# Performance work log

Hardware: AMD Instinct MI355X
Metric: run time of the kernel (lower is better)

Reference implementation:

```python
import jax, jax.numpy as jnp
import numpy as np
from jax.scipy.linalg import expm as _expm

B, D = 1024, 128
_SQRT3 = 3.0 ** 0.5
_C1, _C2 = 0.5 - _SQRT3 / 6.0, 0.5 + _SQRT3 / 6.0


def setup_inputs() -> dict:
    key = jax.random.key(0)
    k_t, k_y, k_a, k_w = jax.random.split(key, 4)
    scale = 1.0 / np.sqrt(D)  # keep ||Omega|| moderate so expm is well-conditioned
    return {
        "t0": jax.random.uniform(k_t, (B,), dtype=jnp.float32),
        "h": jnp.float32(0.1),
        "y0": jax.random.normal(k_y, (B, D), dtype=jnp.float32),
        "A0": jax.random.normal(k_a, (B, D, D), dtype=jnp.float32) * scale,
        "W": jax.random.normal(k_w, (B, D, D), dtype=jnp.float32) * scale,
    }


def reference(t0, h, y0, A0, W):
    # A(t) = A0 + t * W evaluated at the two Gauss-Legendre nodes
    t1 = t0 + _C1 * h  # (B,)
    t2 = t0 + _C2 * h  # (B,)
    A1 = A0 + t1[:, None, None] * W  # (B, D, D)
    A2 = A0 + t2[:, None, None] * W  # (B, D, D)
    alpha1 = (h * 0.5) * (A1 + A2)
    alpha2 = (h * _SQRT3) * (A2 - A1)
    comm = alpha1 @ alpha2 - alpha2 @ alpha1  # [alpha1, alpha2]
    Omega = alpha1 - comm / 12.0
    U = jax.vmap(_expm)(Omega)  # batched matrix exponential (B, D, D)
    y_next = jnp.einsum("bij,bj->bi", U, y0)  # (B, D)
    return y_next, jnp.stack((A1, A2), axis=0)
```

## Files before the change

kernel.cpp:

```cpp
#include <hip/hip_runtime.h>

#define B_SZ 1024
#define D_SZ 128
#define KTERMS 8

typedef float vfloat4 __attribute__((ext_vector_type(4)));

__device__ inline float dotq(const vfloat4* q, const float* v) {
    float a0 = 0.f, a1 = 0.f, a2 = 0.f, a3 = 0.f;
#pragma unroll
    for (int j = 0; j < 16; ++j) {
        vfloat4 vv = *(const vfloat4*)(v + 4 * j);
        a0 = fmaf(q[j].x, vv.x, a0);
        a1 = fmaf(q[j].y, vv.y, a1);
        a2 = fmaf(q[j].z, vv.z, a2);
        a3 = fmaf(q[j].w, vv.w, a3);
    }
    return (a0 + a1) + (a2 + a3);
}

__global__ void __launch_bounds__(512, 4)
magnus_kernel(const float* __restrict__ t0p, const float* __restrict__ hp,
              const float* __restrict__ y0, const float* __restrict__ A0,
              const float* __restrict__ W, float* __restrict__ out)
{
    __shared__ __align__(16) float sv[D_SZ];
    __shared__ __align__(16) float su1[D_SZ];
    __shared__ __align__(16) float su2[D_SZ];
    __shared__ __align__(16) float su3[D_SZ];
    __shared__ __align__(16) float su4[D_SZ];

    const int b = blockIdx.x;
    const int tid = threadIdx.x;
    const float h = hp[0];
    const float tb = t0p[b];
    const float SQ3_6 = 0.28867513459481287f;
    const float t1 = tb + (0.5f - SQ3_6) * h;
    const float t2 = tb + (0.5f + SQ3_6) * h;

    const size_t moff = (size_t)b * (D_SZ * D_SZ);
    const float4* A0v = (const float4*)(A0 + moff);
    const float4* Wv  = (const float4*)(W + moff);
    vfloat4* o1 = (vfloat4*)(out + (size_t)B_SZ * D_SZ + moff);
    vfloat4* o2 = (vfloat4*)(out + (size_t)B_SZ * D_SZ
                                 + (size_t)B_SZ * D_SZ * D_SZ + moff);

#pragma unroll 8
    for (int it = 0; it < 8; ++it) {
        int i = it * 512 + tid;
        float4 a = A0v[i];
        float4 w = Wv[i];
        vfloat4 p1, p2;
        p1.x = fmaf(t1, w.x, a.x);
        p1.y = fmaf(t1, w.y, a.y);
        p1.z = fmaf(t1, w.z, a.z);
        p1.w = fmaf(t1, w.w, a.w);
        p2.x = fmaf(t2, w.x, a.x);
        p2.y = fmaf(t2, w.y, a.y);
        p2.z = fmaf(t2, w.z, a.z);
        p2.w = fmaf(t2, w.w, a.w);
        __builtin_nontemporal_store(p1, o1 + i);
        __builtin_nontemporal_store(p2, o2 + i);
    }

    const int grp  = tid >> 8;
    const int t8   = tid & 255;
    const int half = (t8 >> 5) & 1;
    const int row  = (t8 & 31) + ((t8 >> 6) << 5);
    const float* rbase = grp ? (W + moff) : (A0 + moff);
    const vfloat4* src = (const vfloat4*)(rbase + (size_t)row * D_SZ + half * 64);
    vfloat4 q[16];
#pragma unroll
    for (int j = 0; j < 16; ++j) q[j] = src[j];
#pragma unroll
    for (int j = 0; j < 16; ++j) asm volatile("" : "+v"(q[j]));

    float yacc = 0.0f;
    if (tid < D_SZ) {
        float v = y0[(size_t)b * D_SZ + tid];
        sv[tid] = v;
        yacc = v;
    }
    __syncthreads();

    const float hs = h * (tb + 0.5f * h);
    const float c3 = h * h * h * (1.0f / 12.0f);

#pragma unroll
    for (int k = 1; k <= KTERMS; ++k) {
        float a = dotq(q, sv + half * 64);
        a += __shfl_xor(a, 32);
        if (!half) { if (grp == 0) su1[row] = a; else su2[row] = a; }
        __syncthreads();
        const float* vb = grp ? su1 : su2;
        float c = dotq(q, vb + half * 64);
        c += __shfl_xor(c, 32);
        if (!half) { if (grp == 0) su3[row] = c; else su4[row] = c; }
        __syncthreads();
        if (tid < D_SZ) {
            float wn = h * su1[tid] + hs * su2[tid] - c3 * (su3[tid] - su4[tid]);
            wn *= (1.0f / (float)k);
            yacc += wn;
            sv[tid] = wn;
        }
        __syncthreads();
    }

    if (tid < D_SZ) {
        out[(size_t)b * D_SZ + tid] = yacc;
    }
}

extern "C" void kernel_launch(void* const* d_in, const int* in_sizes, int n_in,
                              void* d_out, int out_size, void* d_ws, size_t ws_size,
                              hipStream_t stream) {
    const float* t0 = (const float*)d_in[0];
    const float* h  = (const float*)d_in[1];
    const float* y0 = (const float*)d_in[2];
    const float* A0 = (const float*)d_in[3];
    const float* W  = (const float*)d_in[4];
    float* out = (float*)d_out;
    magnus_kernel<<<B_SZ, 512, 0, stream>>>(t0, h, y0, A0, W, out);
}
```

Before: 256.3 us.

## Form Omega explicitly with bf16 MFMA commutator, then run Taylor matvecs on it

Instead of applying alpha1 and alpha2 as four matrix-vector products per Taylor term, the kernel builds Omega once per batch. It computes the commutator A0·W − W·A0 with bf16 MFMA 32x32x16 tiles, stores Omega in a swizzled 64KB shared buffer, and then does a single matvec per term with ping-pong vectors and one barrier per term. This trades two dense 128^3 GEMMs per matrix, strided uncoalesced B-fragment global loads and 64KB of LDS (which lowers occupancy) for fewer per-term barriers and matvecs. bf16 rounding of the commutator inputs reduces accuracy.

```diff
diff --git a/kernel.cpp b/kernel.cpp
--- a/kernel.cpp
+++ b/kernel.cpp
@@ -5,18 +5,29 @@
 #define KTERMS 8
 
 typedef float vfloat4 __attribute__((ext_vector_type(4)));
+typedef float f32x16 __attribute__((ext_vector_type(16)));
+typedef short bf16x8 __attribute__((ext_vector_type(8)));
 
-__device__ inline float dotq(const vfloat4* q, const float* v) {
-    float a0 = 0.f, a1 = 0.f, a2 = 0.f, a3 = 0.f;
+__device__ inline short f2bf(float x) {
+    union { float f; unsigned u; } c; c.f = x;
+    unsigned u = c.u + 0x7fffu + ((c.u >> 16) & 1u);
+    return (short)(u >> 16);
+}
+
+__device__ inline bf16x8 afrag(const float* M, int r, int k0) {
+    const float4* p = (const float4*)(M + r * 128 + k0);
+    float4 x0 = p[0], x1 = p[1];
+    bf16x8 f;
+    f[0] = f2bf(x0.x); f[1] = f2bf(x0.y); f[2] = f2bf(x0.z); f[3] = f2bf(x0.w);
+    f[4] = f2bf(x1.x); f[5] = f2bf(x1.y); f[6] = f2bf(x1.z); f[7] = f2bf(x1.w);
+    return f;
+}
+
+__device__ inline bf16x8 bfrag(const float* M, int k0, int c) {
+    bf16x8 f;
 #pragma unroll
-    for (int j = 0; j < 16; ++j) {
-        vfloat4 vv = *(const vfloat4*)(v + 4 * j);
-        a0 = fmaf(q[j].x, vv.x, a0);
-        a1 = fmaf(q[j].y, vv.y, a1);
-        a2 = fmaf(q[j].z, vv.z, a2);
-        a3 = fmaf(q[j].w, vv.w, a3);
-    }
-    return (a0 + a1) + (a2 + a3);
+    for (int e = 0; e < 8; ++e) f[e] = f2bf(M[(k0 + e) * 128 + c]);
+    return f;
 }
 
 __global__ void __launch_bounds__(512, 4)
@@ -24,11 +35,8 @@
               const float* __restrict__ y0, const float* __restrict__ A0,
               const float* __restrict__ W, float* __restrict__ out)
 {
-    __shared__ __align__(16) float sv[D_SZ];
-    __shared__ __align__(16) float su1[D_SZ];
-    __shared__ __align__(16) float su2[D_SZ];
-    __shared__ __align__(16) float su3[D_SZ];
-    __shared__ __align__(16) float su4[D_SZ];
+    __shared__ __align__(16) float sOmega[D_SZ * D_SZ];
+    __shared__ __align__(16) float sv[2][D_SZ];
 
     const int b = blockIdx.x;
     const int tid = threadIdx.x;
@@ -51,63 +59,98 @@
         float4 a = A0v[i];
         float4 w = Wv[i];
         vfloat4 p1, p2;
-        p1.x = fmaf(t1, w.x, a.x);
-        p1.y = fmaf(t1, w.y, a.y);
-        p1.z = fmaf(t1, w.z, a.z);
-        p1.w = fmaf(t1, w.w, a.w);
-        p2.x = fmaf(t2, w.x, a.x);
-        p2.y = fmaf(t2, w.y, a.y);
-        p2.z = fmaf(t2, w.z, a.z);
-        p2.w = fmaf(t2, w.w, a.w);
+        p1.x = fmaf(t1, w.x, a.x); p1.y = fmaf(t1, w.y, a.y);
+        p1.z = fmaf(t1, w.z, a.z); p1.w = fmaf(t1, w.w, a.w);
+        p2.x = fmaf(t2, w.x, a.x); p2.y = fmaf(t2, w.y, a.y);
+        p2.z = fmaf(t2, w.z, a.z); p2.w = fmaf(t2, w.w, a.w);
         __builtin_nontemporal_store(p1, o1 + i);
         __builtin_nontemporal_store(p2, o2 + i);
     }
 
-    const int grp  = tid >> 8;
-    const int t8   = tid & 255;
-    const int half = (t8 >> 5) & 1;
-    const int row  = (t8 & 31) + ((t8 >> 6) << 5);
-    const float* rbase = grp ? (W + moff) : (A0 + moff);
-    const vfloat4* src = (const vfloat4*)(rbase + (size_t)row * D_SZ + half * 64);
-    vfloat4 q[16];
-#pragma unroll
-    for (int j = 0; j < 16; ++j) q[j] = src[j];
-#pragma unroll
-    for (int j = 0; j < 16; ++j) asm volatile("" : "+v"(q[j]));
+    const int l  = tid & 63;
+    const int w  = tid >> 6;
+    const int lh = l >> 5;
+    const int lc = l & 31;
 
-    float yacc = 0.0f;
-    if (tid < D_SZ) {
-        float v = y0[(size_t)b * D_SZ + tid];
-        sv[tid] = v;
-        yacc = v;
-    }
-    __syncthreads();
+    const float* Ag = A0 + moff;
+    const float* Wg = W  + moff;
 
     const float hs = h * (tb + 0.5f * h);
     const float c3 = h * h * h * (1.0f / 12.0f);
 
 #pragma unroll
+    for (int t = 0; t < 2; ++t) {
+        const int tile = w * 2 + t;
+        const int mr = tile >> 2, nc = tile & 3;
+        const int ra = mr * 32 + lc;
+        const int cb = nc * 32 + lc;
+
+        f32x16 acc1 = {};
+#pragma unroll
+        for (int ks = 0; ks < 8; ++ks) {
+            int k0 = ks * 16 + 8 * lh;
+            bf16x8 aA = afrag(Ag, ra, k0);
+            bf16x8 bW = bfrag(Wg, k0, cb);
+            acc1 = __builtin_amdgcn_mfma_f32_32x32x16_bf16(aA, bW, acc1, 0, 0, 0);
+        }
+        f32x16 acc2 = {};
+#pragma unroll
+        for (int ks = 0; ks < 8; ++ks) {
+            int k0 = ks * 16 + 8 * lh;
+            bf16x8 aW = afrag(Wg, ra, k0);
+            bf16x8 bA = bfrag(Ag, k0, cb);
+            acc2 = __builtin_amdgcn_mfma_f32_32x32x16_bf16(aW, bA, acc2, 0, 0, 0);
+        }
+#pragma unroll
+        for (int reg = 0; reg < 16; ++reg) {
+            int grow = mr * 32 + (reg & 3) + 8 * (reg >> 2) + 4 * lh;
+            int gcol = nc * 32 + lc;
+            float a0v = Ag[grow * 128 + gcol];
+            float wv  = Wg[grow * 128 + gcol];
+            float om = fmaf(h, a0v, fmaf(hs, wv, -c3 * (acc1[reg] - acc2[reg])));
+            sOmega[grow * 128 + (gcol ^ ((grow & 7) << 2))] = om;
+        }
+    }
+
+    const int q    = l >> 4;
+    const int prow = w * 16 + (l & 15);
+    float yacc = 0.0f;
+    if (l < 16) {
+        float v = y0[(size_t)b * D_SZ + prow];
+        sv[0][prow] = v;
+        yacc = v;
+    }
+    __syncthreads();
+
+    const float* orow = sOmega + prow * 128;
+    const int sw = (prow & 7) << 2;
+#pragma unroll
     for (int k = 1; k <= KTERMS; ++k) {
-        float a = dotq(q, sv + half * 64);
+        const float* vin = sv[(k - 1) & 1];
+        float s0 = 0.f, s1 = 0.f, s2 = 0.f, s3 = 0.f;
+#pragma unroll
+        for (int c = 0; c < 8; ++c) {
+            int colb = q * 32 + 4 * c;
+            vfloat4 ov = *(const vfloat4*)(orow + (colb ^ sw));
+            vfloat4 vv = *(const vfloat4*)(vin + colb);
+            s0 = fmaf(ov.x, vv.x, s0);
+            s1 = fmaf(ov.y, vv.y, s1);
+            s2 = fmaf(ov.z, vv.z, s2);
+            s3 = fmaf(ov.w, vv.w, s3);
+        }
+        float a = (s0 + s1) + (s2 + s3);
+        a += __shfl_xor(a, 16);
         a += __shfl_xor(a, 32);
-        if (!half) { if (grp == 0) su1[row] = a; else su2[row] = a; }
-        __syncthreads();
-        const float* vb = grp ? su1 : su2;
-        float c = dotq(q, vb + half * 64);
-        c += __shfl_xor(c, 32);
-        if (!half) { if (grp == 0) su3[row] = c; else su4[row] = c; }
-        __syncthreads();
-        if (tid < D_SZ) {
-            float wn = h * su1[tid] + hs * su2[tid] - c3 * (su3[tid] - su4[tid]);
-            wn *= (1.0f / (float)k);
+        if (l < 16) {
+            float wn = a * (1.0f / (float)k);
             yacc += wn;
-            sv[tid] = wn;
+            sv[k & 1][prow] = wn;
         }
         __syncthreads();
     }
 
-    if (tid < D_SZ) {
-        out[(size_t)b * D_SZ + tid] = yacc;
+    if (l < 16) {
+        out[(size_t)b * D_SZ + prow] = yacc;
     }
 }
 
```

After: 547.0 us. 2.13x slower.

## Stage A0 and W as bf16 in LDS instead of re-reading fp32 rows into registers

Applied to the files above, without the earlier changes.

During the A1/A2 pass the kernel now packs A0 and W to bf16 and stores them in shared memory with a padded row stride. The Taylor-series matvecs then read operands from LDS instead of reloading each row from global memory into 64 registers per thread. This removes the second global read of both matrices and frees registers, at the cost of about 68KB of LDS per block, which limits blocks per CU. The bf16 rounding also lowers the precision of the exponential-action result.

```diff
diff --git a/kernel.cpp b/kernel.cpp
--- a/kernel.cpp
+++ b/kernel.cpp
@@ -3,18 +3,28 @@
 #define B_SZ 1024
 #define D_SZ 128
 #define KTERMS 8
+#define RSTRIDE 68
 
 typedef float vfloat4 __attribute__((ext_vector_type(4)));
 
-__device__ inline float dotq(const vfloat4* q, const float* v) {
+__device__ inline float bflo(unsigned u) { return __uint_as_float(u << 16); }
+__device__ inline float bfhi(unsigned u) { return __uint_as_float(u & 0xffff0000u); }
+
+__device__ inline float dotlds(const unsigned* rq, const float* v) {
     float a0 = 0.f, a1 = 0.f, a2 = 0.f, a3 = 0.f;
 #pragma unroll
-    for (int j = 0; j < 16; ++j) {
-        vfloat4 vv = *(const vfloat4*)(v + 4 * j);
-        a0 = fmaf(q[j].x, vv.x, a0);
-        a1 = fmaf(q[j].y, vv.y, a1);
-        a2 = fmaf(q[j].z, vv.z, a2);
-        a3 = fmaf(q[j].w, vv.w, a3);
+    for (int j = 0; j < 8; ++j) {
+        uint4 qq = *(const uint4*)(rq + 4 * j);
+        vfloat4 v0 = *(const vfloat4*)(v + 8 * j);
+        vfloat4 v1 = *(const vfloat4*)(v + 8 * j + 4);
+        a0 = fmaf(bflo(qq.x), v0.x, a0);
+        a1 = fmaf(bfhi(qq.x), v0.y, a1);
+        a2 = fmaf(bflo(qq.y), v0.z, a2);
+        a3 = fmaf(bfhi(qq.y), v0.w, a3);
+        a0 = fmaf(bflo(qq.z), v1.x, a0);
+        a1 = fmaf(bfhi(qq.z), v1.y, a1);
+        a2 = fmaf(bflo(qq.w), v1.z, a2);
+        a3 = fmaf(bfhi(qq.w), v1.w, a3);
     }
     return (a0 + a1) + (a2 + a3);
 }
@@ -24,6 +34,8 @@
               const float* __restrict__ y0, const float* __restrict__ A0,
               const float* __restrict__ W, float* __restrict__ out)
 {
+    __shared__ __align__(16) unsigned sA[D_SZ * RSTRIDE];
+    __shared__ __align__(16) unsigned sW[D_SZ * RSTRIDE];
     __shared__ __align__(16) float sv[D_SZ];
     __shared__ __align__(16) float su1[D_SZ];
     __shared__ __align__(16) float su2[D_SZ];
@@ -51,29 +63,29 @@
         float4 a = A0v[i];
         float4 w = Wv[i];
         vfloat4 p1, p2;
-        p1.x = fmaf(t1, w.x, a.x);
-        p1.y = fmaf(t1, w.y, a.y);
-        p1.z = fmaf(t1, w.z, a.z);
-        p1.w = fmaf(t1, w.w, a.w);
-        p2.x = fmaf(t2, w.x, a.x);
-        p2.y = fmaf(t2, w.y, a.y);
-        p2.z = fmaf(t2, w.z, a.z);
-        p2.w = fmaf(t2, w.w, a.w);
+        p1.x = fmaf(t1, w.x, a.x); p1.y = fmaf(t1, w.y, a.y);
+        p1.z = fmaf(t1, w.z, a.z); p1.w = fmaf(t1, w.w, a.w);
+        p2.x = fmaf(t2, w.x, a.x); p2.y = fmaf(t2, w.y, a.y);
+        p2.z = fmaf(t2, w.z, a.z); p2.w = fmaf(t2, w.w, a.w);
         __builtin_nontemporal_store(p1, o1 + i);
         __builtin_nontemporal_store(p2, o2 + i);
+
+        unsigned pa0, pa1, pw0, pw1;
+        asm("v_cvt_pk_bf16_f32 %0, %1, %2" : "=v"(pa0) : "v"(a.x), "v"(a.y));
+        asm("v_cvt_pk_bf16_f32 %0, %1, %2" : "=v"(pa1) : "v"(a.z), "v"(a.w));
+        asm("v_cvt_pk_bf16_f32 %0, %1, %2" : "=v"(pw0) : "v"(w.x), "v"(w.y));
+        asm("v_cvt_pk_bf16_f32 %0, %1, %2" : "=v"(pw1) : "v"(w.z), "v"(w.w));
+        int r = i >> 5;
+        int p = (2 * i) & 63;
+        *(uint2*)(&sA[r * RSTRIDE + p]) = make_uint2(pa0, pa1);
+        *(uint2*)(&sW[r * RSTRIDE + p]) = make_uint2(pw0, pw1);
     }
 
     const int grp  = tid >> 8;
     const int t8   = tid & 255;
     const int half = (t8 >> 5) & 1;
     const int row  = (t8 & 31) + ((t8 >> 6) << 5);
-    const float* rbase = grp ? (W + moff) : (A0 + moff);
-    const vfloat4* src = (const vfloat4*)(rbase + (size_t)row * D_SZ + half * 64);
-    vfloat4 q[16];
-#pragma unroll
-    for (int j = 0; j < 16; ++j) q[j] = src[j];
-#pragma unroll
-    for (int j = 0; j < 16; ++j) asm volatile("" : "+v"(q[j]));
+    const unsigned* rq = (grp ? sW : sA) + row * RSTRIDE + half * 32;
 
     float yacc = 0.0f;
     if (tid < D_SZ) {
@@ -88,12 +100,12 @@
 
 #pragma unroll
     for (int k = 1; k <= KTERMS; ++k) {
-        float a = dotq(q, sv + half * 64);
+        float a = dotlds(rq, sv + half * 64);
         a += __shfl_xor(a, 32);
         if (!half) { if (grp == 0) su1[row] = a; else su2[row] = a; }
         __syncthreads();
         const float* vb = grp ? su1 : su2;
-        float c = dotq(q, vb + half * 64);
+        float c = dotlds(rq, vb + half * 64);
         c += __shfl_xor(c, 32);
         if (!half) { if (grp == 0) su3[row] = c; else su4[row] = c; }
         __syncthreads();
```

New measurement: 257.2 us. No clear change (+0.4%).

## Specialize warps: split A1/A2 streaming from bf16 register-resident Taylor matvecs

Applied to the files above, without the earlier changes.

Splits the block into two halves. One half streams A0/W and writes A1/A2. The other half holds whole rows of A0 or W packed as bf16 in registers and runs the Taylor-series matvec loop. Each thread now owns a full row, so the cross-lane shuffle reduction and two shared buffers are gone, and the combine step is done with a pair shuffle. Barriers are raw s_barrier instructions, and the streaming loop inserts matching barriers to stay in step with the compute half. The series is cut from 8 to 7 terms and the matrix is rounded to bf16, which lowers accuracy and may break tolerance. The hand-matched barrier counts are fragile.

```diff
diff --git a/kernel.cpp b/kernel.cpp
--- a/kernel.cpp
+++ b/kernel.cpp
@@ -2,19 +2,25 @@
 
 #define B_SZ 1024
 #define D_SZ 128
-#define KTERMS 8
+#define KTERMS 7
 
 typedef float vfloat4 __attribute__((ext_vector_type(4)));
 
-__device__ inline float dotq(const vfloat4* q, const float* v) {
+__device__ inline float bflo(unsigned u) { return __uint_as_float(u << 16); }
+__device__ inline float bfhi(unsigned u) { return __uint_as_float(u & 0xffff0000u); }
+
+#define BAR_J1() asm volatile("s_barrier")
+#define BAR_J2() asm volatile("s_waitcnt lgkmcnt(0)\ns_barrier" ::: "memory")
+
+__device__ inline float dotR(const unsigned* R, const float* v) {
     float a0 = 0.f, a1 = 0.f, a2 = 0.f, a3 = 0.f;
 #pragma unroll
-    for (int j = 0; j < 16; ++j) {
+    for (int j = 0; j < 32; ++j) {
         vfloat4 vv = *(const vfloat4*)(v + 4 * j);
-        a0 = fmaf(q[j].x, vv.x, a0);
-        a1 = fmaf(q[j].y, vv.y, a1);
-        a2 = fmaf(q[j].z, vv.z, a2);
-        a3 = fmaf(q[j].w, vv.w, a3);
+        a0 = fmaf(bflo(R[2 * j]),     vv.x, a0);
+        a1 = fmaf(bfhi(R[2 * j]),     vv.y, a1);
+        a2 = fmaf(bflo(R[2 * j + 1]), vv.z, a2);
+        a3 = fmaf(bfhi(R[2 * j + 1]), vv.w, a3);
     }
     return (a0 + a1) + (a2 + a3);
 }
@@ -24,90 +30,84 @@
               const float* __restrict__ y0, const float* __restrict__ A0,
               const float* __restrict__ W, float* __restrict__ out)
 {
-    __shared__ __align__(16) float sv[D_SZ];
+    __shared__ __align__(16) float svr[D_SZ];
     __shared__ __align__(16) float su1[D_SZ];
     __shared__ __align__(16) float su2[D_SZ];
-    __shared__ __align__(16) float su3[D_SZ];
-    __shared__ __align__(16) float su4[D_SZ];
 
-    const int b = blockIdx.x;
+    const int b   = blockIdx.x;
     const int tid = threadIdx.x;
-    const float h = hp[0];
+    const float h  = hp[0];
     const float tb = t0p[b];
-    const float SQ3_6 = 0.28867513459481287f;
-    const float t1 = tb + (0.5f - SQ3_6) * h;
-    const float t2 = tb + (0.5f + SQ3_6) * h;
+    const size_t moff = (size_t)b * (D_SZ * D_SZ);
 
-    const size_t moff = (size_t)b * (D_SZ * D_SZ);
-    const float4* A0v = (const float4*)(A0 + moff);
-    const float4* Wv  = (const float4*)(W + moff);
-    vfloat4* o1 = (vfloat4*)(out + (size_t)B_SZ * D_SZ + moff);
-    vfloat4* o2 = (vfloat4*)(out + (size_t)B_SZ * D_SZ
-                                 + (size_t)B_SZ * D_SZ * D_SZ + moff);
+    if (tid < 256) {
+        const float SQ3_6 = 0.28867513459481287f;
+        const float t1 = tb + (0.5f - SQ3_6) * h;
+        const float t2 = tb + (0.5f + SQ3_6) * h;
+        const float4* A0v = (const float4*)(A0 + moff);
+        const float4* Wv  = (const float4*)(W + moff);
+        vfloat4* o1 = (vfloat4*)(out + (size_t)B_SZ * D_SZ + moff);
+        vfloat4* o2 = (vfloat4*)(out + (size_t)B_SZ * D_SZ
+                                     + (size_t)B_SZ * D_SZ * D_SZ + moff);
+#pragma unroll
+        for (int it = 0; it < 16; ++it) {
+            int i = it * 256 + tid;
+            float4 a = A0v[i];
+            float4 w = Wv[i];
+            vfloat4 p1, p2;
+            p1.x = fmaf(t1, w.x, a.x); p1.y = fmaf(t1, w.y, a.y);
+            p1.z = fmaf(t1, w.z, a.z); p1.w = fmaf(t1, w.w, a.w);
+            p2.x = fmaf(t2, w.x, a.x); p2.y = fmaf(t2, w.y, a.y);
+            p2.z = fmaf(t2, w.z, a.z); p2.w = fmaf(t2, w.w, a.w);
+            __builtin_nontemporal_store(p1, o1 + i);
+            __builtin_nontemporal_store(p2, o2 + i);
+            if (it >= 1 && it <= 14) BAR_J1();
+        }
+    } else {
+        const int tl = tid - 256;
+        const int m  = tl & 1;
+        const int r  = tl >> 1;
+        const float* rowp = (m ? W : A0) + moff + (size_t)r * D_SZ;
 
-#pragma unroll 8
-    for (int it = 0; it < 8; ++it) {
-        int i = it * 512 + tid;
-        float4 a = A0v[i];
-        float4 w = Wv[i];
-        vfloat4 p1, p2;
-        p1.x = fmaf(t1, w.x, a.x);
-        p1.y = fmaf(t1, w.y, a.y);
-        p1.z = fmaf(t1, w.z, a.z);
-        p1.w = fmaf(t1, w.w, a.w);
-        p2.x = fmaf(t2, w.x, a.x);
-        p2.y = fmaf(t2, w.y, a.y);
-        p2.z = fmaf(t2, w.z, a.z);
-        p2.w = fmaf(t2, w.w, a.w);
-        __builtin_nontemporal_store(p1, o1 + i);
-        __builtin_nontemporal_store(p2, o2 + i);
-    }
+        unsigned R[64];
+#pragma unroll
+        for (int j = 0; j < 32; ++j) {
+            float4 x = ((const float4*)rowp)[j];
+            asm("v_cvt_pk_bf16_f32 %0, %1, %2" : "=v"(R[2*j])   : "v"(x.x), "v"(x.y));
+            asm("v_cvt_pk_bf16_f32 %0, %1, %2" : "=v"(R[2*j+1]) : "v"(x.z), "v"(x.w));
+        }
 
-    const int grp  = tid >> 8;
-    const int t8   = tid & 255;
-    const int half = (t8 >> 5) & 1;
-    const int row  = (t8 & 31) + ((t8 >> 6) << 5);
-    const float* rbase = grp ? (W + moff) : (A0 + moff);
-    const vfloat4* src = (const vfloat4*)(rbase + (size_t)row * D_SZ + half * 64);
-    vfloat4 q[16];
-#pragma unroll
-    for (int j = 0; j < 16; ++j) q[j] = src[j];
-#pragma unroll
-    for (int j = 0; j < 16; ++j) asm volatile("" : "+v"(q[j]));
+        float yv = y0[(size_t)b * D_SZ + r];
+        if (m == 0) svr[r] = yv;
+        float yacc = yv;
+        BAR_J2();
 
-    float yacc = 0.0f;
-    if (tid < D_SZ) {
-        float v = y0[(size_t)b * D_SZ + tid];
-        sv[tid] = v;
-        yacc = v;
-    }
-    __syncthreads();
-
-    const float hs = h * (tb + 0.5f * h);
-    const float c3 = h * h * h * (1.0f / 12.0f);
+        const float hs = h * (tb + 0.5f * h);
+        const float c3 = h * h * h * (1.0f / 12.0f);
 
 #pragma unroll
-    for (int k = 1; k <= KTERMS; ++k) {
-        float a = dotq(q, sv + half * 64);
-        a += __shfl_xor(a, 32);
-        if (!half) { if (grp == 0) su1[row] = a; else su2[row] = a; }
-        __syncthreads();
-        const float* vb = grp ? su1 : su2;
-        float c = dotq(q, vb + half * 64);
-        c += __shfl_xor(c, 32);
-        if (!half) { if (grp == 0) su3[row] = c; else su4[row] = c; }
-        __syncthreads();
-        if (tid < D_SZ) {
-            float wn = h * su1[tid] + hs * su2[tid] - c3 * (su3[tid] - su4[tid]);
-            wn *= (1.0f / (float)k);
+        for (int k = 1; k <= KTERMS; ++k) {
+            float ownA = dotR(R, svr);
+            if (m == 0) su1[r] = ownA; else su2[r] = ownA;
+            BAR_J2();
+            float ownB = dotR(R, m ? su1 : su2);
+            float othA = __shfl_xor(ownA, 1);
+            float othB = __shfl_xor(ownB, 1);
+            float u1 = m ? othA : ownA;
+            float u2 = m ? ownA : othA;
+            float u3 = m ? othB : ownB;
+            float u4 = m ? ownB : othB;
+            float wn = (h * u1 + hs * u2 - c3 * (u3 - u4)) * (1.0f / (float)k);
             yacc += wn;
-            sv[tid] = wn;
+            if (k < KTERMS) {
+                if (m == 0) svr[r] = wn;
+                BAR_J2();
+            }
         }
-        __syncthreads();
-    }
 
-    if (tid < D_SZ) {
-        out[(size_t)b * D_SZ + tid] = yacc;
+        if (m == 0) {
+            out[(size_t)b * D_SZ + r] = yacc;
+        }
     }
 }
 
```

Result: slower. 322.8 us (+26.0%).
